# Kernel tuning notes

Hardware: AMD Instinct MI355X
Metric: run time of the kernel (lower is better)

Reference implementation:

```python
import jax, jax.numpy as jnp
import numpy as np

T, B = 64, 1024
DETER, STOC, EMB, ACT, MLP = 512, 64, 1024, 6, 512
MIN_STD = 0.1


def setup_inputs() -> dict:
    key = jax.random.key(0)
    ks = jax.random.split(key, 20)

    def lin(k, fan_in, fan_out):
        return jax.random.normal(k, (fan_in, fan_out), jnp.float32) / np.sqrt(fan_in)

    inp = {
        "actions": jax.random.normal(ks[0], (T, B, ACT), jnp.float32),
        "nonterminals": jnp.ones((T, B, 1), jnp.float32),
        "obs_embeddings": jax.random.normal(ks[1], (T, B, EMB), jnp.float32),
        "init_deter": jnp.zeros((B, DETER), jnp.float32),
        "init_stoc": jax.random.uniform(ks[2], (B, STOC), jnp.float32),
        "noise_prior": jax.random.uniform(ks[3], (T, B, STOC), jnp.float32),
        "noise_post": jax.random.uniform(ks[4], (T, B, STOC), jnp.float32),
        # fc_input
        "Wi": lin(ks[5], STOC + ACT, DETER),
        "bi": jnp.zeros((DETER,), jnp.float32),
        # GRUCell (torch layout: [3H, in], gate order r, z, n)
        "W_ih": jax.random.normal(ks[6], (3 * DETER, DETER), jnp.float32) / np.sqrt(DETER),
        "W_hh": jax.random.normal(ks[7], (3 * DETER, DETER), jnp.float32) / np.sqrt(DETER),
        "b_ih": jnp.zeros((3 * DETER,), jnp.float32),
        "b_hh": jnp.zeros((3 * DETER,), jnp.float32),
        # fc_prior
        "Wp1": lin(ks[8], DETER, MLP),
        "bp1": jnp.zeros((MLP,), jnp.float32),
        "Wp2": lin(ks[9], MLP, 2 * STOC),
        "bp2": jnp.zeros((2 * STOC,), jnp.float32),
        # fc_posterior
        "Wq1": lin(ks[10], DETER + EMB, MLP),
        "bq1": jnp.zeros((MLP,), jnp.float32),
        "Wq2": lin(ks[11], MLP, 2 * STOC),
        "bq2": jnp.zeros((2 * STOC,), jnp.float32),
    }
    return inp


def _rollout(actions, nonterminals, obs_embeddings, init_deter, init_stoc,
             noise_prior, noise_post, Wi, bi, W_ih, W_hh, b_ih, b_hh,
             Wp1, bp1, Wp2, bp2, Wq1, bq1, Wq2, bq2):
    def step(carry, inp):
        deter, stoc = carry
        a, nt, emb, eps_p, eps_q = inp
        # fc_input: Linear + ELU
        x = jax.nn.elu(jnp.concatenate([stoc * nt, a], axis=-1) @ Wi + bi)
        h = deter * nt
        # torch GRUCell
        gi = x @ W_ih.T + b_ih
        gh = h @ W_hh.T + b_hh
        ir, iz, inn = jnp.split(gi, 3, axis=-1)
        hr, hz, hn = jnp.split(gh, 3, axis=-1)
        r = jax.nn.sigmoid(ir + hr)
        z = jax.nn.sigmoid(iz + hz)
        n = jnp.tanh(inn + r * hn)
        deter_new = (1.0 - z) * n + z * h
        # prior head
        pr = jax.nn.elu(deter_new @ Wp1 + bp1) @ Wp2 + bp2
        pm, ps = jnp.split(pr, 2, axis=-1)
        ps = jax.nn.softplus(ps) + MIN_STD
        pstoc = pm + ps * eps_p  # uniform noise, as in RSSMState (torch.rand_like)
        # posterior head
        po = jax.nn.elu(jnp.concatenate([deter_new, emb], axis=-1) @ Wq1 + bq1) @ Wq2 + bq2
        qm, qs = jnp.split(po, 2, axis=-1)
        qs = jax.nn.softplus(qs) + MIN_STD
        qstoc = qm + qs * eps_q
        out = jnp.concatenate([deter_new, pm, ps, pstoc, qm, qs, qstoc], axis=-1)
        return (deter_new, qstoc), out

    _, outs = jax.lax.scan(step, (init_deter, init_stoc),
                           (actions, nonterminals, obs_embeddings, noise_prior, noise_post))
    return outs  # [T, B, DETER + 6*STOC]


def reference(actions, nonterminals, obs_embeddings, init_deter, init_stoc,
              noise_prior, noise_post, Wi, bi, W_ih, W_hh, b_ih, b_hh,
              Wp1, bp1, Wp2, bp2, Wq1, bq1, Wq2, bq2):
    return _rollout(actions, nonterminals, obs_embeddings, init_deter, init_stoc,
                    noise_prior, noise_post, Wi, bi, W_ih, W_hh, b_ih, b_hh,
                    Wp1, bp1, Wp2, bp2, Wq1, bq1, Wq2, bq2)
```

## Files before the change

kernel.cpp:

```cpp
#include <hip/hip_runtime.h>
#include <hip/hip_bf16.h>
#include <cstdint>

#define T_STEPS 64
#define BATCH   1024
#define DETER   512
#define STOC    64
#define EMB     1024
#define G3      1536
#define OUTD    896

#define DI __device__ __forceinline__

typedef __attribute__((ext_vector_type(8))) short bf8;
typedef __attribute__((ext_vector_type(4))) float f4;

DI float bf2f(short s) {
  union { uint32_t u; float f; } v; v.u = ((uint32_t)(uint16_t)s) << 16; return v.f;
}
DI short f2bf(float f) {
  union { float f; uint32_t u; } v; v.f = f;
  uint32_t r = (v.u + 0x7fffu + ((v.u >> 16) & 1u)) >> 16;
  return (short)(uint16_t)r;
}
DI float elu_f(float x)      { return x > 0.f ? x : expm1f(x); }
DI float sigm(float x)       { return 1.f / (1.f + expf(-x)); }
DI float softplus_f(float x) { return fmaxf(x, 0.f) + log1pf(expf(-fabsf(x))); }

DI bool is_f32(const void* nt) { return ((const uint32_t*)nt)[0] == 0x3F800000u; }
DI float gld(const void* p, size_t i, bool f) {
  return f ? ((const float*)p)[i] : bf2f(((const short*)p)[i]);
}
DI void gst(void* p, size_t i, float v, bool f) {
  if (f) ((float*)p)[i] = v; else ((short*)p)[i] = f2bf(v);
}

template<int BM, int BN, int WM, bool AF32, typename EPI>
DI void gemm_core(const void* Av, int lda, const short* Bp, int ldb, int K,
                  int m0, int n0, char* smem, int tid, EPI&& epi)
{
  constexpr int WN = 4 / WM;
  constexpr int SM = BM / 16 / WM;
  constexpr int SN = BN / 16 / WN;
  short* As = (short*)smem;
  short* Bs = As + BM * 32;
  int wave = tid >> 6, lane = tid & 63;
  int arow = (wave % WM) * (SM * 16), brow = (wave / WM) * (SN * 16);

  f4 acc[SM][SN] = {};

  for (int k0 = 0; k0 < K; k0 += 32) {
#pragma unroll
    for (int it = 0; it < (BM * 4) / 256; ++it) {
      int idx = it * 256 + tid;
      int r = idx >> 2, kc = (idx & 3) << 3;
      if (AF32) {
        const float* s = (const float*)Av + (size_t)(m0 + r) * lda + k0 + kc;
        f4 lo = *(const f4*)s, hi = *(const f4*)(s + 4);
        bf8 v;
#pragma unroll
        for (int j = 0; j < 4; ++j) { v[j] = f2bf(lo[j]); v[4 + j] = f2bf(hi[j]); }
        *(bf8*)&As[idx * 8] = v;
      } else {
        *(bf8*)&As[idx * 8] =
            *(const bf8*)((const short*)Av + (size_t)(m0 + r) * lda + k0 + kc);
      }
    }
#pragma unroll
    for (int it = 0; it < (BN * 4) / 256; ++it) {
      int idx = it * 256 + tid;
      int r = idx >> 2, kc = (idx & 3) << 3;
      *(bf8*)&Bs[idx * 8] = *(const bf8*)&Bp[(size_t)(n0 + r) * ldb + k0 + kc];
    }
    __syncthreads();

    bf8 af[SM], bfr[SN];
#pragma unroll
    for (int s = 0; s < SM; ++s)
      af[s] = *(const bf8*)&As[(arow + s * 16 + (lane & 15)) * 32 + ((lane >> 4) << 3)];
#pragma unroll
    for (int s = 0; s < SN; ++s)
      bfr[s] = *(const bf8*)&Bs[(brow + s * 16 + (lane & 15)) * 32 + ((lane >> 4) << 3)];
#pragma unroll
    for (int sm = 0; sm < SM; ++sm)
#pragma unroll
      for (int sn = 0; sn < SN; ++sn)
        acc[sm][sn] = __builtin_amdgcn_mfma_f32_16x16x32_bf16(af[sm], bfr[sn], acc[sm][sn], 0, 0, 0);
    __syncthreads();
  }
  epi(acc, m0 + arow, n0 + brow, lane);
}

__global__ __launch_bounds__(256) void k_prep(
    const void* __restrict__ Wi,  const void* __restrict__ Wp1,
    const void* __restrict__ Wq1, const void* __restrict__ Wp2,
    const void* __restrict__ Wq2, const void* __restrict__ Wih,
    const void* __restrict__ Whh, const void* __restrict__ nt,
    short* __restrict__ WiT, short* __restrict__ WpT, short* __restrict__ WqT,
    short* __restrict__ Wp2T, short* __restrict__ Wq2T,
    short* __restrict__ Wihc, short* __restrict__ Whhc)
{
  bool f = is_f32(nt);
  int idx = blockIdx.x * 256 + threadIdx.x;
  if (idx < 512 * 96) {
    int n = idx / 96, k = idx % 96;
    WiT[idx] = (k < 70) ? f2bf(gld(Wi, (size_t)k * 512 + n, f)) : (short)0;
    return;
  }
  idx -= 512 * 96;
  if (idx < 512 * 512) {
    int n = idx >> 9, k = idx & 511;
    WpT[idx] = f2bf(gld(Wp1, (size_t)k * 512 + n, f));
    return;
  }
  idx -= 512 * 512;
  if (idx < 512 * 1536) {
    int n = idx / 1536, k = idx % 1536;
    WqT[idx] = f2bf(gld(Wq1, (size_t)k * 512 + n, f));
    return;
  }
  idx -= 512 * 1536;
  if (idx < 128 * 512) {
    int n = idx >> 9, k = idx & 511;
    Wp2T[idx] = f2bf(gld(Wp2, (size_t)k * 128 + n, f));
    return;
  }
  idx -= 128 * 512;
  if (idx < 128 * 512) {
    int n = idx >> 9, k = idx & 511;
    Wq2T[idx] = f2bf(gld(Wq2, (size_t)k * 128 + n, f));
    return;
  }
  idx -= 128 * 512;
  if (idx < G3 * 512) { Wihc[idx] = f2bf(gld(Wih, idx, f)); return; }
  idx -= G3 * 512;
  if (idx < G3 * 512) { Whhc[idx] = f2bf(gld(Whh, idx, f)); }
}

__global__ __launch_bounds__(256) void k_init(
    const void* __restrict__ init_deter, const void* __restrict__ init_stoc,
    const void* __restrict__ nt, const void* __restrict__ actions,
    short* __restrict__ Ax, short* __restrict__ hbf, float* __restrict__ hf32)
{
  bool f = is_f32(nt);
  int idx = blockIdx.x * 256 + threadIdx.x;
  if (idx < BATCH * 96) {
    int b = idx / 96, k = idx % 96;
    float nt0 = gld(nt, b, f);
    float v;
    if (k < 64)      v = gld(init_stoc, (size_t)b * 64 + k, f) * nt0;
    else if (k < 70) v = gld(actions, (size_t)b * 6 + (k - 64), f);
    else             v = 0.f;
    Ax[idx] = f2bf(v);
  } else {
    int j = idx - BATCH * 96;
    if (j < BATCH * DETER) {
      int b = j >> 9;
      float v = gld(init_deter, j, f) * gld(nt, b, f);
      hbf[j]  = f2bf(v);
      hf32[j] = v;
    }
  }
}

__global__ __launch_bounds__(256) void k_phase1(
    const short* __restrict__ Ax, const short* __restrict__ WiT, const void* __restrict__ bi,
    const short* __restrict__ hbf, const short* __restrict__ Whhc, const void* __restrict__ bhh,
    const void* __restrict__ emb, int t, const short* __restrict__ WqT,
    const void* __restrict__ nt,
    short* __restrict__ x, short* __restrict__ gh, short* __restrict__ hq2)
{
  extern __shared__ char smem[];
  bool f = is_f32(nt);
  int tid = threadIdx.x, b = blockIdx.x;
  if (b < 32) {
    int m0 = (b >> 2) * 128, n0 = (b & 3) * 128;
    gemm_core<128, 128, 2, false>(Ax, 96, WiT, 96, 96, m0, n0, smem, tid,
      [&](auto& acc, int rb, int cb, int lane) {
        int q = lane >> 4, li = lane & 15;
#pragma unroll
        for (int sm = 0; sm < 4; ++sm)
#pragma unroll
          for (int sn = 0; sn < 4; ++sn)
#pragma unroll
            for (int i = 0; i < 4; ++i) {
              int r = rb + sm * 16 + q * 4 + i, c = cb + sn * 16 + li;
              x[(size_t)r * 512 + c] = f2bf(elu_f(acc[sm][sn][i] + gld(bi, c, f)));
            }
      });
  } else if (b < 224) {
    int r = b - 32;
    int m0 = (r / 24) * 128, n0 = (r % 24) * 64;
    gemm_core<128, 64, 2, false>(hbf, 512, Whhc, 512, 512, m0, n0, smem, tid,
      [&](auto& acc, int rb, int cb, int lane) {
        int q = lane >> 4, li = lane & 15;
#pragma unroll
        for (int sm = 0; sm < 4; ++sm)
#pragma unroll
          for (int sn = 0; sn < 2; ++sn)
#pragma unroll
            for (int i = 0; i < 4; ++i) {
              int rr = rb + sm * 16 + q * 4 + i, c = cb + sn * 16 + li;
              gh[(size_t)rr * G3 + c] = f2bf(acc[sm][sn][i] + gld(bhh, c, f));
            }
      });
  } else {
    int r = b - 224;
    int m0 = (r / 8) * 64, n0 = (r % 8) * 64;
    size_t eoff = (size_t)t * BATCH * EMB;
    auto epi = [&](auto& acc, int rb, int cb, int lane) {
      int q = lane >> 4, li = lane & 15;
#pragma unroll
      for (int sm = 0; sm < 2; ++sm)
#pragma unroll
        for (int sn = 0; sn < 2; ++sn)
#pragma unroll
          for (int i = 0; i < 4; ++i) {
            int rr = rb + sm * 16 + q * 4 + i, c = cb + sn * 16 + li;
            hq2[(size_t)rr * 512 + c] = f2bf(acc[sm][sn][i]);
          }
    };
    if (f) gemm_core<64, 64, 2, true >((const void*)((const float*)emb + eoff), 1024,
                                       WqT + 512, 1536, 1024, m0, n0, smem, tid, epi);
    else   gemm_core<64, 64, 2, false>((const void*)((const short*)emb + eoff), 1024,
                                       WqT + 512, 1536, 1024, m0, n0, smem, tid, epi);
  }
}

__global__ __launch_bounds__(256) void k_gru(
    const short* __restrict__ x, const short* __restrict__ Wihc, const void* __restrict__ bih,
    const short* __restrict__ gh, const void* __restrict__ nt, int t,
    short* __restrict__ hbf, float* __restrict__ hf32,
    short* __restrict__ dbf, void* __restrict__ outv)
{
  extern __shared__ char smem[];
  bool f = is_f32(nt);
  short* As = (short*)smem;
  short* Bs = As + 128 * 32;
  int tid = threadIdx.x, lane = tid & 63, wave = tid >> 6;
  int m0 = (blockIdx.x >> 3) * 128, n0 = (blockIdx.x & 7) * 64;
  int arow = (wave & 1) * 64, brow = (wave >> 1) * 32;

  f4 acc[3][4][2] = {};

  for (int k0 = 0; k0 < 512; k0 += 32) {
#pragma unroll
    for (int it = 0; it < 2; ++it) {
      int idx = it * 256 + tid;
      *(bf8*)&As[idx * 8] = *(const bf8*)&x[(size_t)(m0 + (idx >> 2)) * 512 + k0 + ((idx & 3) << 3)];
    }
#pragma unroll
    for (int g = 0; g < 3; ++g) {
      int idx = tid;
      *(bf8*)&Bs[g * 2048 + idx * 8] =
          *(const bf8*)&Wihc[(size_t)(n0 + g * 512 + (idx >> 2)) * 512 + k0 + ((idx & 3) << 3)];
    }
    __syncthreads();

    bf8 af[4];
#pragma unroll
    for (int s = 0; s < 4; ++s)
      af[s] = *(const bf8*)&As[(arow + s * 16 + (lane & 15)) * 32 + ((lane >> 4) << 3)];
#pragma unroll
    for (int g = 0; g < 3; ++g)
#pragma unroll
      for (int sn = 0; sn < 2; ++sn) {
        bf8 bfr = *(const bf8*)&Bs[g * 2048 + (brow + sn * 16 + (lane & 15)) * 32 + ((lane >> 4) << 3)];
#pragma unroll
        for (int sm = 0; sm < 4; ++sm)
          acc[g][sm][sn] = __builtin_amdgcn_mfma_f32_16x16x32_bf16(af[sm], bfr, acc[g][sm][sn], 0, 0, 0);
      }
    __syncthreads();
  }

  int q = lane >> 4, li = lane & 15;
#pragma unroll
  for (int sm = 0; sm < 4; ++sm)
#pragma unroll
    for (int sn = 0; sn < 2; ++sn)
#pragma unroll
      for (int i = 0; i < 4; ++i) {
        int r = m0 + arow + sm * 16 + q * 4 + i;
        int c = n0 + brow + sn * 16 + li;
        float ir  = acc[0][sm][sn][i] + gld(bih, c, f);
        float iz  = acc[1][sm][sn][i] + gld(bih, 512 + c, f);
        float in_ = acc[2][sm][sn][i] + gld(bih, 1024 + c, f);
        size_t gb = (size_t)r * G3;
        float hr = bf2f(gh[gb + c]);
        float hz = bf2f(gh[gb + 512 + c]);
        float hn = bf2f(gh[gb + 1024 + c]);
        float h  = hf32[(size_t)r * 512 + c];
        float rr = sigm(ir + hr);
        float zz = sigm(iz + hz);
        float nn = tanhf(in_ + rr * hn);
        float dn = (1.f - zz) * nn + zz * h;
        gst(outv, ((size_t)t * BATCH + r) * OUTD + c, dn, f);
        dbf[(size_t)r * 512 + c] = f2bf(dn);
        if (t < T_STEPS - 1) {
          float hv = dn * gld(nt, (size_t)(t + 1) * BATCH + r, f);
          hbf[(size_t)r * 512 + c]  = f2bf(hv);
          hf32[(size_t)r * 512 + c] = hv;
        }
      }
}

__global__ __launch_bounds__(256) void k_phase4(
    const short* __restrict__ dbf, const short* __restrict__ WpT, const void* __restrict__ bp1,
    const short* __restrict__ WqT, const void* __restrict__ bq1,
    const short* __restrict__ hq2, const void* __restrict__ nt,
    short* __restrict__ hp, short* __restrict__ hq)
{
  extern __shared__ char smem[];
  bool f = is_f32(nt);
  int tid = threadIdx.x, b = blockIdx.x;
  if (b < 64) {
    int m0 = (b / 8) * 128, n0 = (b % 8) * 64;
    gemm_core<128, 64, 2, false>(dbf, 512, WpT, 512, 512, m0, n0, smem, tid,
      [&](auto& acc, int rb, int cb, int lane) {
        int q = lane >> 4, li = lane & 15;
#pragma unroll
        for (int sm = 0; sm < 4; ++sm)
#pragma unroll
          for (int sn = 0; sn < 2; ++sn)
#pragma unroll
            for (int i = 0; i < 4; ++i) {
              int rr = rb + sm * 16 + q * 4 + i, c = cb + sn * 16 + li;
              hp[(size_t)rr * 512 + c] = f2bf(elu_f(acc[sm][sn][i] + gld(bp1, c, f)));
            }
      });
  } else {
    int r = b - 64;
    int m0 = (r / 8) * 128, n0 = (r % 8) * 64;
    gemm_core<128, 64, 2, false>(dbf, 512, WqT, 1536, 512, m0, n0, smem, tid,
      [&](auto& acc, int rb, int cb, int lane) {
        int q = lane >> 4, li = lane & 15;
#pragma unroll
        for (int sm = 0; sm < 4; ++sm)
#pragma unroll
          for (int sn = 0; sn < 2; ++sn)
#pragma unroll
            for (int i = 0; i < 4; ++i) {
              int rr = rb + sm * 16 + q * 4 + i, c = cb + sn * 16 + li;
              float v = acc[sm][sn][i] + bf2f(hq2[(size_t)rr * 512 + c]) + gld(bq1, c, f);
              hq[(size_t)rr * 512 + c] = f2bf(elu_f(v));
            }
      });
  }
}

__global__ __launch_bounds__(256) void k_heads(
    const short* __restrict__ hp, const short* __restrict__ hq,
    const short* __restrict__ Wp2T, const short* __restrict__ Wq2T,
    const void* __restrict__ bp2, const void* __restrict__ bq2,
    const void* __restrict__ noise_p, const void* __restrict__ noise_q,
    const void* __restrict__ nt, const void* __restrict__ actions, int t,
    void* __restrict__ outv, short* __restrict__ Ax)
{
  extern __shared__ char smem[];
  bool f = is_f32(nt);
  int tid = threadIdx.x;
  int head = blockIdx.x & 1;
  int bm   = blockIdx.x >> 1;
  const short* Asrc = head ? hq : hp;
  const short* Bsrc = head ? Wq2T : Wp2T;
  const void* b2    = head ? bq2 : bp2;
  const void* eps   = head ? noise_q : noise_p;
  int obase = head ? 704 : 512;

  gemm_core<64, 128, 4, false>(Asrc, 512, Bsrc, 512, 512, bm * 64, 0, smem, tid,
    [&](auto& acc, int rb, int cb, int lane) {
      int q = lane >> 4, li = lane & 15;
      (void)cb;
#pragma unroll
      for (int sn = 0; sn < 4; ++sn)
#pragma unroll
        for (int i = 0; i < 4; ++i) {
          int r = rb + q * 4 + i;
          int c = sn * 16 + li;
          float m  = acc[0][sn][i]     + gld(b2, c, f);
          float sp = acc[0][sn + 4][i] + gld(b2, 64 + c, f);
          float s  = softplus_f(sp) + 0.1f;
          float e  = gld(eps, ((size_t)t * BATCH + r) * 64 + c, f);
          float st = m + s * e;
          size_t ob = ((size_t)t * BATCH + r) * OUTD + obase;
          gst(outv, ob + c,       m,  f);
          gst(outv, ob + 64 + c,  s,  f);
          gst(outv, ob + 128 + c, st, f);
          if (head && t < T_STEPS - 1)
            Ax[(size_t)r * 96 + c] = f2bf(st * gld(nt, (size_t)(t + 1) * BATCH + r, f));
        }
    });

  if (head == 0 && t < T_STEPS - 1) {
    for (int idx = tid; idx < 64 * 32; idx += 256) {
      int r = bm * 64 + (idx >> 5);
      int c = 64 + (idx & 31);
      float v = (c < 70) ? gld(actions, ((size_t)(t + 1) * BATCH + r) * 6 + (c - 64), f) : 0.f;
      Ax[(size_t)r * 96 + c] = f2bf(v);
    }
  }
}

extern "C" void kernel_launch(void* const* d_in, const int* in_sizes, int n_in,
                              void* d_out, int out_size, void* d_ws, size_t ws_size,
                              hipStream_t stream)
{
  const void* actions    = d_in[0];
  const void* nonterm    = d_in[1];
  const void* emb        = d_in[2];
  const void* init_deter = d_in[3];
  const void* init_stoc  = d_in[4];
  const void* noise_p    = d_in[5];
  const void* noise_q    = d_in[6];
  const void* Wi  = d_in[7];
  const void* bi  = d_in[8];
  const void* Wih = d_in[9];
  const void* Whh = d_in[10];
  const void* bih = d_in[11];
  const void* bhh = d_in[12];
  const void* Wp1 = d_in[13];
  const void* bp1 = d_in[14];
  const void* Wp2 = d_in[15];
  const void* bp2 = d_in[16];
  const void* Wq1 = d_in[17];
  const void* bq1 = d_in[18];
  const void* Wq2 = d_in[19];
  const void* bq2 = d_in[20];

  char* ws = (char*)d_ws;
  short* WiT  = (short*)(ws + 0);
  short* WpT  = (short*)(ws + 98304);
  short* WqT  = (short*)(ws + 622592);
  short* Wp2T = (short*)(ws + 2195456);
  short* Wq2T = (short*)(ws + 2326528);
  short* Wihc = (short*)(ws + 2457600);
  short* Whhc = (short*)(ws + 4030464);
  short* Ax   = (short*)(ws + 5603328);
  short* x    = (short*)(ws + 5799936);
  short* dbf  = (short*)(ws + 6848512);
  short* hbf  = (short*)(ws + 7897088);
  short* hp   = (short*)(ws + 8945664);
  short* hq   = (short*)(ws + 9994240);
  short* gh   = (short*)(ws + 11042816);
  short* hq2  = (short*)(ws + 14188544);
  float* hf32 = (float*)(ws + 15237120);

  (void)in_sizes; (void)n_in; (void)out_size;
  if (ws_size < 17334272) return;

  k_prep<<<10944, 256, 0, stream>>>(Wi, Wp1, Wq1, Wp2, Wq2, Wih, Whh, nonterm,
                                    WiT, WpT, WqT, Wp2T, Wq2T, Wihc, Whhc);
  k_init<<<2432, 256, 0, stream>>>(init_deter, init_stoc, nonterm, actions, Ax, hbf, hf32);

  for (int t = 0; t < T_STEPS; ++t) {
    k_phase1<<<352, 256, 16384, stream>>>(Ax, WiT, bi, hbf, Whhc, bhh, emb, t, WqT,
                                          nonterm, x, gh, hq2);
    k_gru<<<64, 256, 20480, stream>>>(x, Wihc, bih, gh, nonterm, t, hbf, hf32, dbf, d_out);
    k_phase4<<<128, 256, 12288, stream>>>(dbf, WpT, bp1, WqT, bq1, hq2, nonterm, hp, hq);
    k_heads<<<32, 256, 12288, stream>>>(hp, hq, Wp2T, Wq2T, bp2, bq2,
                                        noise_p, noise_q, nonterm, actions, t, d_out, Ax);
  }
}
```

Baseline: 7.658 ms.

## Fuse whole recurrent rollout into one persistent kernel with batch-row blocks

Replaces the four launches per timestep with a single persistent kernel. Each of 128 blocks owns 8 batch rows and runs all 64 steps, keeping the hidden state, intermediate activations and stochastic input in swizzled LDS, while streaming weights straight from global or L2 into MFMA. The time-independent embedding projection for the posterior is optionally precomputed for all timesteps in one large GEMM when the workspace is big enough. This removes 256 launches and the global round trips between them, but it uses only 128 blocks with M=8 rows padded into 16-row MFMA tiles, so half of each tile is wasted. Every step also re-reads the full weight set from cache.

```diff
diff --git a/kernel.cpp b/kernel.cpp
--- a/kernel.cpp
+++ b/kernel.cpp
@@ -1,5 +1,4 @@
 #include <hip/hip_runtime.h>
-#include <hip/hip_bf16.h>
 #include <cstdint>
 
 #define T_STEPS 64
@@ -10,6 +9,10 @@
 #define G3      1536
 #define OUTD    896
 
+#define ROWS 8
+#define NB2  128
+#define TH2  512
+
 #define DI __device__ __forceinline__
 
 typedef __attribute__((ext_vector_type(8))) short bf8;
@@ -33,6 +36,264 @@
 }
 DI void gst(void* p, size_t i, float v, bool f) {
   if (f) ((float*)p)[i] = v; else ((short*)p)[i] = f2bf(v);
+}
+
+#define SWZ(off, r) ((off) ^ (((r) & 7) << 4))
+
+#define OFF_PO   0
+#define OFF_AXL  8192
+#define OFF_EMA  0
+#define OFF_XA   16384
+#define OFF_HA   24576
+#define OFF_DNA  32768
+#define OFF_HPA  40960
+#define OFF_HQA  49152
+#define OFF_H2L  57344
+#define SM_BYTES 65536
+
+struct P2 {
+  const void *actions, *nonterm, *emb;
+  const void *bi, *bih, *bhh, *bp1, *bp2, *bq1, *bq2, *noise_p, *noise_q;
+  const short *WiT, *WpT, *WqT, *Wp2T, *Wq2T, *Wihc, *Whhc, *Ax0;
+  const short *hbf;
+  const float *hf32;
+  const short *hq2g;
+  void *outv;
+};
+
+template<int NT, int NKI>
+DI void g16(const char* Alds, int apitch, int akoffB, const short* B, int ldb,
+            const int* rows, int lane, f4* acc)
+{
+  int q = lane >> 4, li = lane & 15;
+  const short* bp[NT];
+#pragma unroll
+  for (int u = 0; u < NT; ++u) bp[u] = B + (size_t)(rows[u] + li) * ldb + q * 8;
+  int ab = li * apitch + akoffB + q * 16;
+  int sw = (li & 7) << 4;
+#pragma unroll 4
+  for (int k = 0; k < NKI; ++k) {
+    bf8 af = *(const bf8*)(Alds + ((ab + k * 64) ^ sw));
+#pragma unroll
+    for (int u = 0; u < NT; ++u) {
+      bf8 bv = *(const bf8*)(bp[u] + k * 32);
+      acc[u] = __builtin_amdgcn_mfma_f32_16x16x32_bf16(af, bv, acc[u], 0, 0, 0);
+    }
+  }
+}
+
+__global__ __launch_bounds__(TH2, 2) void k_roll2(P2 P)
+{
+  __shared__ __align__(16) char sm[SM_BYTES];
+  bool f = is_f32(P.nonterm);
+  const bool pre = (P.hq2g != nullptr);
+  int tid = threadIdx.x;
+  int wave = tid >> 6, lane = tid & 63, q = lane >> 4, li = lane & 15;
+  int r0 = blockIdx.x * ROWS;
+
+  {
+    int r = tid >> 6, k8 = tid & 63;
+    bf8 v = *(const bf8*)&P.hbf[(size_t)(r0 + r) * 512 + k8 * 8];
+    *(bf8*)(sm + OFF_HA + SWZ(r * 1024 + k8 * 16, r)) = v;
+  }
+  float hreg[4][4];
+#pragma unroll
+  for (int s = 0; s < 4; ++s) {
+    int c = 64 * wave + 16 * s + li;
+#pragma unroll
+    for (int i = 0; i < 4; ++i) {
+      int r = 4 * q + i;
+      hreg[s][i] = (r < ROWS) ? P.hf32[(size_t)(r0 + r) * 512 + c] : 0.f;
+    }
+  }
+  if (tid < 96) {
+    int r = tid / 12, k8 = tid % 12;
+    bf8 v = *(const bf8*)&P.Ax0[(size_t)(r0 + r) * 96 + k8 * 8];
+    *(bf8*)(sm + OFF_AXL + SWZ(r * 256 + k8 * 16, r)) = v;
+  }
+  __syncthreads();
+
+  auto xgemm = [&]() {
+    f4 ax[4] = {};
+    int rx[4];
+#pragma unroll
+    for (int s2 = 0; s2 < 4; ++s2) rx[s2] = 64 * wave + 16 * s2;
+    g16<4, 3>(sm + OFF_AXL, 256, 0, P.WiT, 96, rx, lane, ax);
+#pragma unroll
+    for (int s2 = 0; s2 < 4; ++s2) {
+      int c = 64 * wave + 16 * s2 + li;
+#pragma unroll
+      for (int i = 0; i < 4; ++i) {
+        int r = 4 * q + i;
+        if (r < ROWS)
+          *(short*)(sm + OFF_XA + SWZ(r * 1024 + c * 2, r)) =
+              f2bf(elu_f(ax[s2][i] + gld(P.bi, c, f)));
+      }
+    }
+  };
+  xgemm();
+  __syncthreads();
+
+  for (int t = 0; t < T_STEPS; ++t) {
+    if (!pre) {
+      for (int ci = tid; ci < ROWS * 128; ci += TH2) {
+        int r = ci >> 7, k8 = ci & 127;
+        bf8 v;
+        if (f) {
+          const float* s = (const float*)P.emb + ((size_t)t * BATCH + r0 + r) * EMB + k8 * 8;
+          f4 lo = *(const f4*)s, hi = *(const f4*)(s + 4);
+#pragma unroll
+          for (int j = 0; j < 4; ++j) { v[j] = f2bf(lo[j]); v[4 + j] = f2bf(hi[j]); }
+        } else {
+          v = *(const bf8*)((const short*)P.emb + ((size_t)t * BATCH + r0 + r) * EMB + k8 * 8);
+        }
+        *(bf8*)(sm + OFF_EMA + SWZ(r * 2048 + k8 * 16, r)) = v;
+      }
+      __syncthreads();
+      f4 ah[4] = {};
+      int rh[4];
+#pragma unroll
+      for (int s = 0; s < 4; ++s) rh[s] = 64 * wave + 16 * s;
+      g16<4, 32>(sm + OFF_EMA, 2048, 0, P.WqT + 512, 1536, rh, lane, ah);
+#pragma unroll
+      for (int s = 0; s < 4; ++s) {
+        int c = 64 * wave + 16 * s + li;
+#pragma unroll
+        for (int i = 0; i < 4; ++i) {
+          int r = 4 * q + i;
+          if (r < ROWS)
+            *(short*)(sm + OFF_H2L + SWZ(r * 1024 + c * 2, r)) = f2bf(ah[s][i]);
+        }
+      }
+    }
+
+    f4 acc[16] = {};
+    {
+      int rows12[12];
+#pragma unroll
+      for (int u = 0; u < 12; ++u)
+        rows12[u] = (u >> 2) * 512 + 64 * wave + 16 * (u & 3);
+      g16<12, 16>(sm + OFF_HA, 1024, 0, P.Whhc, 512, rows12, lane, acc);
+      g16<8, 16>(sm + OFF_XA, 1024, 0, P.Wihc, 512, rows12, lane, acc);
+      int rowsn[4];
+#pragma unroll
+      for (int s = 0; s < 4; ++s) rowsn[s] = 1024 + 64 * wave + 16 * s;
+      g16<4, 16>(sm + OFF_XA, 1024, 0, P.Wihc, 512, rowsn, lane, acc + 12);
+    }
+    __syncthreads();
+
+#pragma unroll
+    for (int s = 0; s < 4; ++s) {
+      int c = 64 * wave + 16 * s + li;
+      float br = gld(P.bih, c, f) + gld(P.bhh, c, f);
+      float bz = gld(P.bih, 512 + c, f) + gld(P.bhh, 512 + c, f);
+      float bni = gld(P.bih, 1024 + c, f);
+      float bnh = gld(P.bhh, 1024 + c, f);
+#pragma unroll
+      for (int i = 0; i < 4; ++i) {
+        int r = 4 * q + i;
+        if (r < ROWS) {
+          float rr = sigm(acc[s][i] + br);
+          float zz = sigm(acc[4 + s][i] + bz);
+          float hn = acc[8 + s][i] + bnh;
+          float nn = tanhf(acc[12 + s][i] + bni + rr * hn);
+          float dn = (1.f - zz) * nn + zz * hreg[s][i];
+          gst(P.outv, ((size_t)t * BATCH + r0 + r) * OUTD + c, dn, f);
+          *(short*)(sm + OFF_DNA + SWZ(r * 1024 + c * 2, r)) = f2bf(dn);
+          if (t < T_STEPS - 1) {
+            float hv = dn * gld(P.nonterm, (size_t)(t + 1) * BATCH + r0 + r, f);
+            hreg[s][i] = hv;
+            *(short*)(sm + OFF_HA + SWZ(r * 1024 + c * 2, r)) = f2bf(hv);
+          }
+        }
+      }
+    }
+    __syncthreads();
+
+    {
+      f4 ap[8] = {};
+      int pc0 = 128 * wave;
+      int rows8[8];
+#pragma unroll
+      for (int u = 0; u < 8; ++u) rows8[u] = (wave < 4 ? pc0 : pc0 - 512) + 16 * u;
+      if (wave < 4) g16<8, 16>(sm + OFF_DNA, 1024, 0, P.WpT, 512, rows8, lane, ap);
+      else          g16<8, 16>(sm + OFF_DNA, 1024, 0, P.WqT, 1536, rows8, lane, ap);
+#pragma unroll
+      for (int u = 0; u < 8; ++u) {
+        int c = pc0 + 16 * u + li;
+#pragma unroll
+        for (int i = 0; i < 4; ++i) {
+          int r = 4 * q + i;
+          if (r < ROWS) {
+            float v;
+            if (wave < 4) {
+              v = ap[u][i] + gld(P.bp1, c, f);
+              *(short*)(sm + OFF_HPA + SWZ(r * 1024 + c * 2, r)) = f2bf(elu_f(v));
+            } else {
+              int cc = c - 512;
+              v = ap[u][i] + gld(P.bq1, cc, f);
+              v += pre ? bf2f(P.hq2g[((size_t)t * BATCH + r0 + r) * 512 + cc])
+                       : bf2f(*(const short*)(sm + OFF_H2L + SWZ(r * 1024 + cc * 2, r)));
+              *(short*)(sm + OFF_HQA + SWZ(r * 1024 + cc * 2, r)) = f2bf(elu_f(v));
+            }
+          }
+        }
+      }
+    }
+    __syncthreads();
+
+    {
+      f4 ah2[2] = {};
+      int hc0 = 32 * (wave & 3);
+      int rows2[2] = { hc0, hc0 + 16 };
+      if (wave < 4) g16<2, 16>(sm + OFF_HPA, 1024, 0, P.Wp2T, 512, rows2, lane, ah2);
+      else          g16<2, 16>(sm + OFF_HQA, 1024, 0, P.Wq2T, 512, rows2, lane, ah2);
+      float* po = (float*)(sm + OFF_PO);
+#pragma unroll
+      for (int u = 0; u < 2; ++u)
+#pragma unroll
+        for (int i = 0; i < 4; ++i) {
+          int r = 4 * q + i;
+          if (r < ROWS)
+            po[r * 256 + (wave < 4 ? 0 : 128) + hc0 + 16 * u + li] = ah2[u][i];
+        }
+    }
+    __syncthreads();
+
+    {
+      const float* po = (const float*)(sm + OFF_PO);
+      int r = (tid >> 6) & 7, c = tid & 63;
+#pragma unroll
+      for (int head = 0; head < 2; ++head) {
+        const void* b2 = head ? P.bq2 : P.bp2;
+        float m  = po[r * 256 + head * 128 + c]      + gld(b2, c, f);
+        float sp = po[r * 256 + head * 128 + 64 + c] + gld(b2, 64 + c, f);
+        float s = softplus_f(sp) + 0.1f;
+        float e = gld(head ? P.noise_q : P.noise_p, ((size_t)t * BATCH + r0 + r) * 64 + c, f);
+        float st = m + s * e;
+        size_t ob = ((size_t)t * BATCH + r0 + r) * OUTD + (head ? 704 : 512);
+        gst(P.outv, ob + c,       m,  f);
+        gst(P.outv, ob + 64 + c,  s,  f);
+        gst(P.outv, ob + 128 + c, st, f);
+        if (head && t < T_STEPS - 1) {
+          float nt1 = gld(P.nonterm, (size_t)(t + 1) * BATCH + r0 + r, f);
+          *(short*)(sm + OFF_AXL + SWZ(r * 256 + c * 2, r)) = f2bf(st * nt1);
+        }
+      }
+    }
+
+    if (t < T_STEPS - 1) {
+      if (tid < 256) {
+        int r = tid >> 5, c = 64 + (tid & 31);
+        float v = (c < 70)
+            ? gld(P.actions, ((size_t)(t + 1) * BATCH + r0 + r) * 6 + (c - 64), f) : 0.f;
+        *(short*)(sm + OFF_AXL + SWZ(r * 256 + c * 2, r)) = f2bf(v);
+      }
+      __syncthreads();
+      xgemm();
+      __syncthreads();
+    }
+  }
 }
 
 template<int BM, int BN, int WM, bool AF32, typename EPI>
@@ -82,13 +343,38 @@
     for (int s = 0; s < SN; ++s)
       bfr[s] = *(const bf8*)&Bs[(brow + s * 16 + (lane & 15)) * 32 + ((lane >> 4) << 3)];
 #pragma unroll
-    for (int sm = 0; sm < SM; ++sm)
+    for (int sm2 = 0; sm2 < SM; ++sm2)
 #pragma unroll
       for (int sn = 0; sn < SN; ++sn)
-        acc[sm][sn] = __builtin_amdgcn_mfma_f32_16x16x32_bf16(af[sm], bfr[sn], acc[sm][sn], 0, 0, 0);
+        acc[sm2][sn] = __builtin_amdgcn_mfma_f32_16x16x32_bf16(af[sm2], bfr[sn], acc[sm2][sn], 0, 0, 0);
     __syncthreads();
   }
   epi(acc, m0 + arow, n0 + brow, lane);
+}
+
+__global__ __launch_bounds__(256) void k_hq2(const void* __restrict__ emb,
+                                             const short* __restrict__ WqT,
+                                             const void* __restrict__ nt,
+                                             short* __restrict__ hq2g)
+{
+  extern __shared__ char smem[];
+  bool f = is_f32(nt);
+  int tid = threadIdx.x;
+  int m0 = (blockIdx.x >> 2) * 128, n0 = (blockIdx.x & 3) * 128;
+  auto epi = [&](auto& acc, int rb, int cb, int lane) {
+    int q = lane >> 4, li = lane & 15;
+#pragma unroll
+    for (int sm2 = 0; sm2 < 4; ++sm2)
+#pragma unroll
+      for (int sn = 0; sn < 4; ++sn)
+#pragma unroll
+        for (int i = 0; i < 4; ++i) {
+          int r = rb + sm2 * 16 + q * 4 + i, c = cb + sn * 16 + li;
+          hq2g[(size_t)r * 512 + c] = f2bf(acc[sm2][sn][i]);
+        }
+  };
+  if (f) gemm_core<128, 128, 2, true >(emb, 1024, WqT + 512, 1536, 1024, m0, n0, smem, tid, epi);
+  else   gemm_core<128, 128, 2, false>(emb, 1024, WqT + 512, 1536, 1024, m0, n0, smem, tid, epi);
 }
 
 __global__ __launch_bounds__(256) void k_prep(
@@ -159,244 +445,6 @@
       float v = gld(init_deter, j, f) * gld(nt, b, f);
       hbf[j]  = f2bf(v);
       hf32[j] = v;
-    }
-  }
-}
-
-__global__ __launch_bounds__(256) void k_phase1(
-    const short* __restrict__ Ax, const short* __restrict__ WiT, const void* __restrict__ bi,
-    const short* __restrict__ hbf, const short* __restrict__ Whhc, const void* __restrict__ bhh,
-    const void* __restrict__ emb, int t, const short* __restrict__ WqT,
-    const void* __restrict__ nt,
-    short* __restrict__ x, short* __restrict__ gh, short* __restrict__ hq2)
-{
-  extern __shared__ char smem[];
-  bool f = is_f32(nt);
-  int tid = threadIdx.x, b = blockIdx.x;
-  if (b < 32) {
-    int m0 = (b >> 2) * 128, n0 = (b & 3) * 128;
-    gemm_core<128, 128, 2, false>(Ax, 96, WiT, 96, 96, m0, n0, smem, tid,
-      [&](auto& acc, int rb, int cb, int lane) {
-        int q = lane >> 4, li = lane & 15;
-#pragma unroll
-        for (int sm = 0; sm < 4; ++sm)
-#pragma unroll
-          for (int sn = 0; sn < 4; ++sn)
-#pragma unroll
-            for (int i = 0; i < 4; ++i) {
-              int r = rb + sm * 16 + q * 4 + i, c = cb + sn * 16 + li;
-              x[(size_t)r * 512 + c] = f2bf(elu_f(acc[sm][sn][i] + gld(bi, c, f)));
-            }
-      });
-  } else if (b < 224) {
-    int r = b - 32;
-    int m0 = (r / 24) * 128, n0 = (r % 24) * 64;
-    gemm_core<128, 64, 2, false>(hbf, 512, Whhc, 512, 512, m0, n0, smem, tid,
-      [&](auto& acc, int rb, int cb, int lane) {
-        int q = lane >> 4, li = lane & 15;
-#pragma unroll
-        for (int sm = 0; sm < 4; ++sm)
-#pragma unroll
-          for (int sn = 0; sn < 2; ++sn)
-#pragma unroll
-            for (int i = 0; i < 4; ++i) {
-              int rr = rb + sm * 16 + q * 4 + i, c = cb + sn * 16 + li;
-              gh[(size_t)rr * G3 + c] = f2bf(acc[sm][sn][i] + gld(bhh, c, f));
-            }
-      });
-  } else {
-    int r = b - 224;
-    int m0 = (r / 8) * 64, n0 = (r % 8) * 64;
-    size_t eoff = (size_t)t * BATCH * EMB;
-    auto epi = [&](auto& acc, int rb, int cb, int lane) {
-      int q = lane >> 4, li = lane & 15;
-#pragma unroll
-      for (int sm = 0; sm < 2; ++sm)
-#pragma unroll
-        for (int sn = 0; sn < 2; ++sn)
-#pragma unroll
-          for (int i = 0; i < 4; ++i) {
-            int rr = rb + sm * 16 + q * 4 + i, c = cb + sn * 16 + li;
-            hq2[(size_t)rr * 512 + c] = f2bf(acc[sm][sn][i]);
-          }
-    };
-    if (f) gemm_core<64, 64, 2, true >((const void*)((const float*)emb + eoff), 1024,
-                                       WqT + 512, 1536, 1024, m0, n0, smem, tid, epi);
-    else   gemm_core<64, 64, 2, false>((const void*)((const short*)emb + eoff), 1024,
-                                       WqT + 512, 1536, 1024, m0, n0, smem, tid, epi);
-  }
-}
-
-__global__ __launch_bounds__(256) void k_gru(
-    const short* __restrict__ x, const short* __restrict__ Wihc, const void* __restrict__ bih,
-    const short* __restrict__ gh, const void* __restrict__ nt, int t,
-    short* __restrict__ hbf, float* __restrict__ hf32,
-    short* __restrict__ dbf, void* __restrict__ outv)
-{
-  extern __shared__ char smem[];
-  bool f = is_f32(nt);
-  short* As = (short*)smem;
-  short* Bs = As + 128 * 32;
-  int tid = threadIdx.x, lane = tid & 63, wave = tid >> 6;
-  int m0 = (blockIdx.x >> 3) * 128, n0 = (blockIdx.x & 7) * 64;
-  int arow = (wave & 1) * 64, brow = (wave >> 1) * 32;
-
-  f4 acc[3][4][2] = {};
-
-  for (int k0 = 0; k0 < 512; k0 += 32) {
-#pragma unroll
-    for (int it = 0; it < 2; ++it) {
-      int idx = it * 256 + tid;
-      *(bf8*)&As[idx * 8] = *(const bf8*)&x[(size_t)(m0 + (idx >> 2)) * 512 + k0 + ((idx & 3) << 3)];
-    }
-#pragma unroll
-    for (int g = 0; g < 3; ++g) {
-      int idx = tid;
-      *(bf8*)&Bs[g * 2048 + idx * 8] =
-          *(const bf8*)&Wihc[(size_t)(n0 + g * 512 + (idx >> 2)) * 512 + k0 + ((idx & 3) << 3)];
-    }
-    __syncthreads();
-
-    bf8 af[4];
-#pragma unroll
-    for (int s = 0; s < 4; ++s)
-      af[s] = *(const bf8*)&As[(arow + s * 16 + (lane & 15)) * 32 + ((lane >> 4) << 3)];
-#pragma unroll
-    for (int g = 0; g < 3; ++g)
-#pragma unroll
-      for (int sn = 0; sn < 2; ++sn) {
-        bf8 bfr = *(const bf8*)&Bs[g * 2048 + (brow + sn * 16 + (lane & 15)) * 32 + ((lane >> 4) << 3)];
-#pragma unroll
-        for (int sm = 0; sm < 4; ++sm)
-          acc[g][sm][sn] = __builtin_amdgcn_mfma_f32_16x16x32_bf16(af[sm], bfr, acc[g][sm][sn], 0, 0, 0);
-      }
-    __syncthreads();
-  }
-
-  int q = lane >> 4, li = lane & 15;
-#pragma unroll
-  for (int sm = 0; sm < 4; ++sm)
-#pragma unroll
-    for (int sn = 0; sn < 2; ++sn)
-#pragma unroll
-      for (int i = 0; i < 4; ++i) {
-        int r = m0 + arow + sm * 16 + q * 4 + i;
-        int c = n0 + brow + sn * 16 + li;
-        float ir  = acc[0][sm][sn][i] + gld(bih, c, f);
-        float iz  = acc[1][sm][sn][i] + gld(bih, 512 + c, f);
-        float in_ = acc[2][sm][sn][i] + gld(bih, 1024 + c, f);
-        size_t gb = (size_t)r * G3;
-        float hr = bf2f(gh[gb + c]);
-        float hz = bf2f(gh[gb + 512 + c]);
-        float hn = bf2f(gh[gb + 1024 + c]);
-        float h  = hf32[(size_t)r * 512 + c];
-        float rr = sigm(ir + hr);
-        float zz = sigm(iz + hz);
-        float nn = tanhf(in_ + rr * hn);
-        float dn = (1.f - zz) * nn + zz * h;
-        gst(outv, ((size_t)t * BATCH + r) * OUTD + c, dn, f);
-        dbf[(size_t)r * 512 + c] = f2bf(dn);
-        if (t < T_STEPS - 1) {
-          float hv = dn * gld(nt, (size_t)(t + 1) * BATCH + r, f);
-          hbf[(size_t)r * 512 + c]  = f2bf(hv);
-          hf32[(size_t)r * 512 + c] = hv;
-        }
-      }
-}
-
-__global__ __launch_bounds__(256) void k_phase4(
-    const short* __restrict__ dbf, const short* __restrict__ WpT, const void* __restrict__ bp1,
-    const short* __restrict__ WqT, const void* __restrict__ bq1,
-    const short* __restrict__ hq2, const void* __restrict__ nt,
-    short* __restrict__ hp, short* __restrict__ hq)
-{
-  extern __shared__ char smem[];
-  bool f = is_f32(nt);
-  int tid = threadIdx.x, b = blockIdx.x;
-  if (b < 64) {
-    int m0 = (b / 8) * 128, n0 = (b % 8) * 64;
-    gemm_core<128, 64, 2, false>(dbf, 512, WpT, 512, 512, m0, n0, smem, tid,
-      [&](auto& acc, int rb, int cb, int lane) {
-        int q = lane >> 4, li = lane & 15;
-#pragma unroll
-        for (int sm = 0; sm < 4; ++sm)
-#pragma unroll
-          for (int sn = 0; sn < 2; ++sn)
-#pragma unroll
-            for (int i = 0; i < 4; ++i) {
-              int rr = rb + sm * 16 + q * 4 + i, c = cb + sn * 16 + li;
-              hp[(size_t)rr * 512 + c] = f2bf(elu_f(acc[sm][sn][i] + gld(bp1, c, f)));
-            }
-      });
-  } else {
-    int r = b - 64;
-    int m0 = (r / 8) * 128, n0 = (r % 8) * 64;
-    gemm_core<128, 64, 2, false>(dbf, 512, WqT, 1536, 512, m0, n0, smem, tid,
-      [&](auto& acc, int rb, int cb, int lane) {
-        int q = lane >> 4, li = lane & 15;
-#pragma unroll
-        for (int sm = 0; sm < 4; ++sm)
-#pragma unroll
-          for (int sn = 0; sn < 2; ++sn)
-#pragma unroll
-            for (int i = 0; i < 4; ++i) {
-              int rr = rb + sm * 16 + q * 4 + i, c = cb + sn * 16 + li;
-              float v = acc[sm][sn][i] + bf2f(hq2[(size_t)rr * 512 + c]) + gld(bq1, c, f);
-              hq[(size_t)rr * 512 + c] = f2bf(elu_f(v));
-            }
-      });
-  }
-}
-
-__global__ __launch_bounds__(256) void k_heads(
-    const short* __restrict__ hp, const short* __restrict__ hq,
-    const short* __restrict__ Wp2T, const short* __restrict__ Wq2T,
-    const void* __restrict__ bp2, const void* __restrict__ bq2,
-    const void* __restrict__ noise_p, const void* __restrict__ noise_q,
-    const void* __restrict__ nt, const void* __restrict__ actions, int t,
-    void* __restrict__ outv, short* __restrict__ Ax)
-{
-  extern __shared__ char smem[];
-  bool f = is_f32(nt);
-  int tid = threadIdx.x;
-  int head = blockIdx.x & 1;
-  int bm   = blockIdx.x >> 1;
-  const short* Asrc = head ? hq : hp;
-  const short* Bsrc = head ? Wq2T : Wp2T;
-  const void* b2    = head ? bq2 : bp2;
-  const void* eps   = head ? noise_q : noise_p;
-  int obase = head ? 704 : 512;
-
-  gemm_core<64, 128, 4, false>(Asrc, 512, Bsrc, 512, 512, bm * 64, 0, smem, tid,
-    [&](auto& acc, int rb, int cb, int lane) {
-      int q = lane >> 4, li = lane & 15;
-      (void)cb;
-#pragma unroll
-      for (int sn = 0; sn < 4; ++sn)
-#pragma unroll
-        for (int i = 0; i < 4; ++i) {
-          int r = rb + q * 4 + i;
-          int c = sn * 16 + li;
-          float m  = acc[0][sn][i]     + gld(b2, c, f);
-          float sp = acc[0][sn + 4][i] + gld(b2, 64 + c, f);
-          float s  = softplus_f(sp) + 0.1f;
-          float e  = gld(eps, ((size_t)t * BATCH + r) * 64 + c, f);
-          float st = m + s * e;
-          size_t ob = ((size_t)t * BATCH + r) * OUTD + obase;
-          gst(outv, ob + c,       m,  f);
-          gst(outv, ob + 64 + c,  s,  f);
-          gst(outv, ob + 128 + c, st, f);
-          if (head && t < T_STEPS - 1)
-            Ax[(size_t)r * 96 + c] = f2bf(st * gld(nt, (size_t)(t + 1) * BATCH + r, f));
-        }
-    });
-
-  if (head == 0 && t < T_STEPS - 1) {
-    for (int idx = tid; idx < 64 * 32; idx += 256) {
-      int r = bm * 64 + (idx >> 5);
-      int c = 64 + (idx & 31);
-      float v = (c < 70) ? gld(actions, ((size_t)(t + 1) * BATCH + r) * 6 + (c - 64), f) : 0.f;
-      Ax[(size_t)r * 96 + c] = f2bf(v);
     }
   }
 }
@@ -435,29 +483,32 @@
   short* Wq2T = (short*)(ws + 2326528);
   short* Wihc = (short*)(ws + 2457600);
   short* Whhc = (short*)(ws + 4030464);
-  short* Ax   = (short*)(ws + 5603328);
-  short* x    = (short*)(ws + 5799936);
-  short* dbf  = (short*)(ws + 6848512);
-  short* hbf  = (short*)(ws + 7897088);
-  short* hp   = (short*)(ws + 8945664);
-  short* hq   = (short*)(ws + 9994240);
-  short* gh   = (short*)(ws + 11042816);
-  short* hq2  = (short*)(ws + 14188544);
-  float* hf32 = (float*)(ws + 15237120);
+  short* Ax0  = (short*)(ws + 5603328);
+  short* hbf  = (short*)(ws + 5799936);
+  float* hf32 = (float*)(ws + 6848512);
+  short* hq2g = (short*)(ws + 8945664);
 
   (void)in_sizes; (void)n_in; (void)out_size;
-  if (ws_size < 17334272) return;
+  if (ws_size < 8945664) return;
+  bool pre = (ws_size >= 8945664ull + 67108864ull);
 
   k_prep<<<10944, 256, 0, stream>>>(Wi, Wp1, Wq1, Wp2, Wq2, Wih, Whh, nonterm,
                                     WiT, WpT, WqT, Wp2T, Wq2T, Wihc, Whhc);
-  k_init<<<2432, 256, 0, stream>>>(init_deter, init_stoc, nonterm, actions, Ax, hbf, hf32);
-
-  for (int t = 0; t < T_STEPS; ++t) {
-    k_phase1<<<352, 256, 16384, stream>>>(Ax, WiT, bi, hbf, Whhc, bhh, emb, t, WqT,
-                                          nonterm, x, gh, hq2);
-    k_gru<<<64, 256, 20480, stream>>>(x, Wihc, bih, gh, nonterm, t, hbf, hf32, dbf, d_out);
-    k_phase4<<<128, 256, 12288, stream>>>(dbf, WpT, bp1, WqT, bq1, hq2, nonterm, hp, hq);
-    k_heads<<<32, 256, 12288, stream>>>(hp, hq, Wp2T, Wq2T, bp2, bq2,
-                                        noise_p, noise_q, nonterm, actions, t, d_out, Ax);
-  }
-}
+  k_init<<<2432, 256, 0, stream>>>(init_deter, init_stoc, nonterm, actions,
+                                   Ax0, hbf, hf32);
+  if (pre)
+    k_hq2<<<2048, 256, 16384, stream>>>(emb, WqT, nonterm, hq2g);
+
+  P2 P;
+  P.actions = actions; P.nonterm = nonterm; P.emb = emb;
+  P.bi = bi; P.bih = bih; P.bhh = bhh;
+  P.bp1 = bp1; P.bp2 = bp2; P.bq1 = bq1; P.bq2 = bq2;
+  P.noise_p = noise_p; P.noise_q = noise_q;
+  P.WiT = WiT; P.WpT = WpT; P.WqT = WqT; P.Wp2T = Wp2T; P.Wq2T = Wq2T;
+  P.Wihc = Wihc; P.Whhc = Whhc; P.Ax0 = Ax0;
+  P.hbf = hbf; P.hf32 = hf32;
+  P.hq2g = pre ? hq2g : nullptr;
+  P.outv = d_out;
+
+  k_roll2<<<NB2, TH2, 0, stream>>>(P);
+}
```

Measured after the change: 12.67 ms. +65.5%, slower.
